# Optimization experiments

Hardware: AMD Instinct MI355X
Metric: run time of the kernel (lower is better)

## Reference

```python
import jax, jax.numpy as jnp
import numpy as np

T, E, DIM, HID = 8192, 8, 1024, 2048


def setup_inputs() -> dict:
    key = jax.random.key(0)
    k1, k2, k3 = jax.random.split(key, 3)
    x = jax.random.normal(k1, (T, DIM), dtype=jnp.float32)
    w1 = jax.random.normal(k2, (E, HID, DIM), dtype=jnp.float32)
    w2 = jax.random.normal(k3, (E, DIM, HID), dtype=jnp.float32)
    # Tokens are pre-grouped by expert; counts must sum exactly to T.
    num_tokens_per_expert = jnp.full((E,), T // E, dtype=jnp.int32)
    return {"x": x, "w1": w1, "w2": w2, "num_tokens_per_expert": num_tokens_per_expert}


def reference(x, w1, w2, num_tokens_per_expert):
    # Faithful to torch._grouped_mm path: bf16 casts, two ragged grouped GEMMs,
    # result cast back to x.dtype.
    gs = num_tokens_per_expert.astype(jnp.int32)
    xb = x.astype(jnp.bfloat16)                                  # [T, dim]
    w1t = jnp.swapaxes(w1.astype(jnp.bfloat16), -2, -1)          # [E, dim, hid]
    w2t = jnp.swapaxes(w2.astype(jnp.bfloat16), -2, -1)          # [E, hid, dim]
    h = jax.lax.ragged_dot(xb, w1t, gs)                          # [T, hid] bf16
    out = jax.lax.ragged_dot(h, w2t, gs)                         # [T, dim] bf16
    return out.astype(x.dtype)
```

## Files before the change

kernel.cpp:

```cpp
#include <hip/hip_runtime.h>
#include <stdint.h>

#define T_TOK 8192
#define NEXP  8
#define DIMSZ 1024
#define HIDSZ 2048
#define BK    64

typedef __attribute__((ext_vector_type(4))) float f32x4;
typedef __attribute__((ext_vector_type(8))) short s16x8;


__device__ __forceinline__ uint16_t f2bf(float f) {
  uint32_t u = __builtin_bit_cast(uint32_t, f);
  u += 0x7fffu + ((u >> 16) & 1u);
  return (uint16_t)(u >> 16);
}

__device__ __forceinline__ void gload_lds16(const uint16_t* g, const uint16_t* lds_base) {
  __builtin_amdgcn_global_load_lds(
      (const __attribute__((address_space(1))) uint32_t*)(uintptr_t)g,
      (__attribute__((address_space(3))) uint32_t*)(uint32_t)(uintptr_t)lds_base,
      16, 0, 0);
}


__global__ void cvt_all(const float* __restrict__ x, const float* __restrict__ w1,
                        const float* __restrict__ w2, uint16_t* __restrict__ xb,
                        uint16_t* __restrict__ w1b, uint16_t* __restrict__ w2b,
                        const int* __restrict__ counts, int* __restrict__ offs,
                        int* __restrict__ toffs) {
  if (blockIdx.x == 0 && threadIdx.x == 0) {
    int s = 0, ts = 0;
    for (int e = 0; e < NEXP; ++e) {
      offs[e] = s; toffs[e] = ts;
      s += counts[e]; ts += (counts[e] + 127) >> 7;
    }
    offs[NEXP] = s; toffs[NEXP] = ts;
  }
  const int b = blockIdx.x;
  const float4* src; uint4* dst; size_t base;
  if (b < 512)       { src = (const float4*)x;  dst = (uint4*)xb;  base = (size_t)b * 2048; }
  else if (b < 1536) { src = (const float4*)w1; dst = (uint4*)w1b; base = (size_t)(b - 512) * 2048; }
  else               { src = (const float4*)w2; dst = (uint4*)w2b; base = (size_t)(b - 1536) * 2048; }

#pragma unroll
  for (int half = 0; half < 2; ++half) {
    const size_t u0 = base + (size_t)half * 1024 + threadIdx.x;
    float4 v[8];
#pragma unroll
    for (int j = 0; j < 4; ++j) {
      v[2 * j]     = src[2 * (u0 + j * 256)];
      v[2 * j + 1] = src[2 * (u0 + j * 256) + 1];
    }
#pragma unroll
    for (int j = 0; j < 4; ++j) {
      uint4 o;
      o.x = f2bf(v[2 * j].x)     | ((uint32_t)f2bf(v[2 * j].y) << 16);
      o.y = f2bf(v[2 * j].z)     | ((uint32_t)f2bf(v[2 * j].w) << 16);
      o.z = f2bf(v[2 * j + 1].x) | ((uint32_t)f2bf(v[2 * j + 1].y) << 16);
      o.w = f2bf(v[2 * j + 1].z) | ((uint32_t)f2bf(v[2 * j + 1].w) << 16);
      dst[u0 + j * 256] = o;
    }
  }
}

template <bool OUT_BF16>
__global__ __launch_bounds__(256, 4)
void gemm_grouped(const uint16_t* __restrict__ A, const uint16_t* __restrict__ B,
                  void* __restrict__ C, const int* __restrict__ offs,
                  const int* __restrict__ toffs, int N, int K,
                  int mgs, int ntg, int ngx) {
  __shared__ __align__(16) uint16_t As[128 * BK];
  __shared__ __align__(16) uint16_t Bs[128 * BK];

  const int xcd  = blockIdx.x & 7;
  const int slot = blockIdx.x >> 3;
  const int mg = xcd / ngx, ng = xcd % ngx;
  const int mtg = mg * mgs + slot % mgs;
  const int nt  = ng * ntg + slot / mgs;
  if (mtg >= toffs[NEXP]) return;
  int e = 0;
#pragma unroll
  for (int i = 1; i < NEXP; ++i) e += (toffs[i] <= mtg) ? 1 : 0;
  const int mt      = mtg - toffs[e];
  const int m_start = offs[e];
  const int m_count = offs[e + 1] - m_start;
  const int m0      = mt * 128;
  int valid_m = m_count - m0;
  if (valid_m > 128) valid_m = 128;
  const int n0 = nt * 128;

  const int tid  = threadIdx.x;
  const int lane = tid & 63;
  const int w    = tid >> 6;
  const int wm = w & 1, wn = w >> 1;

  const int srow = tid >> 3;
  const int gch  = (tid & 7) ^ (srow & 7);
  const uint16_t* gB = B + (size_t)e * N * K;
  const uint16_t* gA = A + (size_t)m_start * K;

  const uint16_t* aP[4];
  const uint16_t* bP[4];
#pragma unroll
  for (int q = 0; q < 4; ++q) {
    const int rq = q * 32 + srow;
    const int ar = m0 + (rq < valid_m ? rq : valid_m - 1);
    aP[q] = gA + (size_t)ar * K + gch * 8;
    bP[q] = gB + (size_t)(n0 + q * 32 + srow) * K + gch * 8;
  }

  const int fr = lane & 15;
  const int q4 = lane >> 4;
  const int pA0 = ((q4)     ^ (fr & 7)) * 8;
  const int pA1 = ((4 + q4) ^ (fr & 7)) * 8;

  f32x4 acc[4][4];
#pragma unroll
  for (int mi = 0; mi < 4; ++mi)
#pragma unroll
    for (int ni = 0; ni < 4; ++ni) acc[mi][ni] = (f32x4){0.f, 0.f, 0.f, 0.f};

  for (int k0 = 0; k0 < K; k0 += BK) {
    __syncthreads();
#pragma unroll
    for (int q = 0; q < 4; ++q) {
      gload_lds16(aP[q], As + q * 2048 + w * 512);
      gload_lds16(bP[q], Bs + q * 2048 + w * 512);
      aP[q] += BK; bP[q] += BK;
    }
    __syncthreads();

    s16x8 af[4][2], bf[4][2];
#pragma unroll
    for (int mi = 0; mi < 4; ++mi) {
      const int r = (wm * 64 + mi * 16 + fr) * BK;
      af[mi][0] = *(const s16x8*)&As[r + pA0];
      af[mi][1] = *(const s16x8*)&As[r + pA1];
    }
#pragma unroll
    for (int ni = 0; ni < 4; ++ni) {
      const int r = (wn * 64 + ni * 16 + fr) * BK;
      bf[ni][0] = *(const s16x8*)&Bs[r + pA0];
      bf[ni][1] = *(const s16x8*)&Bs[r + pA1];
    }
#pragma unroll
    for (int t = 0; t < 2; ++t)
#pragma unroll
      for (int mi = 0; mi < 4; ++mi)
#pragma unroll
        for (int ni = 0; ni < 4; ++ni)
          acc[mi][ni] = __builtin_amdgcn_mfma_f32_16x16x32_bf16(af[mi][t], bf[ni][t], acc[mi][ni], 0, 0, 0);
  }

  const int cq = (lane >> 4) * 4;
  const int cc = lane & 15;
#pragma unroll
  for (int mi = 0; mi < 4; ++mi) {
#pragma unroll
    for (int r = 0; r < 4; ++r) {
      const int rt = wm * 64 + mi * 16 + cq + r;
      if (rt < valid_m) {
        const size_t rowoff = (size_t)(m_start + m0 + rt) * N;
#pragma unroll
        for (int ni = 0; ni < 4; ++ni) {
          const int col = n0 + wn * 64 + ni * 16 + cc;
          const float v = acc[mi][ni][r];
          if (OUT_BF16) {
            ((uint16_t*)C)[rowoff + col] = f2bf(v);
          } else {
            const uint32_t bb = (uint32_t)f2bf(v) << 16;
            ((float*)C)[rowoff + col] = __builtin_bit_cast(float, bb);
          }
        }
      }
    }
  }
}


extern "C" void kernel_launch(void* const* d_in, const int* in_sizes, int n_in,
                              void* d_out, int out_size, void* d_ws, size_t ws_size,
                              hipStream_t stream) {
  const float* x  = (const float*)d_in[0];
  const float* w1 = (const float*)d_in[1];
  const float* w2 = (const float*)d_in[2];
  const int* cnt  = (const int*)d_in[3];
  float* out = (float*)d_out;

  char* ws = (char*)d_ws;
  uint16_t* xb  = (uint16_t*)(ws);
  uint16_t* w1b = (uint16_t*)(ws + 16777216);
  uint16_t* w2b = (uint16_t*)(ws + 50331648);
  uint16_t* h   = (uint16_t*)(ws + 83886080);
  int* offs     = (int*)(ws + 117440512);
  int* toffs    = offs + 9;

  cvt_all<<<2560, 256, 0, stream>>>(x, w1, w2, xb, w1b, w2b, cnt, offs, toffs);

  gemm_grouped<true><<<8 * 18 * 8, 256, 0, stream>>>(
      xb, w1b, (void*)h, offs, toffs, HIDSZ, DIMSZ, 18, 8, 2);

  gemm_grouped<false><<<8 * 9 * 8, 256, 0, stream>>>(
      h, w2b, (void*)out, offs, toffs, DIMSZ, HIDSZ, 9, 8, 1);
}
```

Baseline: 290.0 us.

## Fuse fp32-to-bf16 weight conversion into grouped GEMM B-tile loads

Result: slower. 316.6 us (+9.2%).

```diff
diff --git a/kernel.cpp b/kernel.cpp
--- a/kernel.cpp
+++ b/kernel.cpp
@@ -17,7 +17,19 @@
   return (uint16_t)(u >> 16);
 }
 
-__device__ __forceinline__ void gload_lds16(const uint16_t* g, const uint16_t* lds_base) {
+#if __has_builtin(__builtin_amdgcn_cvt_pk_bf16_f32)
+typedef __attribute__((ext_vector_type(2))) __bf16 bf16x2;
+__device__ __forceinline__ uint32_t pk2(float a, float b) {
+  bf16x2 r = __builtin_amdgcn_cvt_pk_bf16_f32(a, b);
+  return __builtin_bit_cast(uint32_t, r);
+}
+#else
+__device__ __forceinline__ uint32_t pk2(float a, float b) {
+  return (uint32_t)f2bf(a) | ((uint32_t)f2bf(b) << 16);
+}
+#endif
+
+__device__ __forceinline__ void gload_lds16(const void* g, const void* lds_base) {
   __builtin_amdgcn_global_load_lds(
       (const __attribute__((address_space(1))) uint32_t*)(uintptr_t)g,
       (__attribute__((address_space(3))) uint32_t*)(uint32_t)(uintptr_t)lds_base,
@@ -25,11 +37,9 @@
 }
 
 
-__global__ void cvt_all(const float* __restrict__ x, const float* __restrict__ w1,
-                        const float* __restrict__ w2, uint16_t* __restrict__ xb,
-                        uint16_t* __restrict__ w1b, uint16_t* __restrict__ w2b,
-                        const int* __restrict__ counts, int* __restrict__ offs,
-                        int* __restrict__ toffs) {
+__global__ void cvt_x(const float* __restrict__ x, uint16_t* __restrict__ xb,
+                      const int* __restrict__ counts, int* __restrict__ offs,
+                      int* __restrict__ toffs) {
   if (blockIdx.x == 0 && threadIdx.x == 0) {
     int s = 0, ts = 0;
     for (int e = 0; e < NEXP; ++e) {
@@ -38,12 +48,9 @@
     }
     offs[NEXP] = s; toffs[NEXP] = ts;
   }
-  const int b = blockIdx.x;
-  const float4* src; uint4* dst; size_t base;
-  if (b < 512)       { src = (const float4*)x;  dst = (uint4*)xb;  base = (size_t)b * 2048; }
-  else if (b < 1536) { src = (const float4*)w1; dst = (uint4*)w1b; base = (size_t)(b - 512) * 2048; }
-  else               { src = (const float4*)w2; dst = (uint4*)w2b; base = (size_t)(b - 1536) * 2048; }
-
+  const float4* src = (const float4*)x;
+  uint4* dst = (uint4*)xb;
+  const size_t base = (size_t)blockIdx.x * 2048;
 #pragma unroll
   for (int half = 0; half < 2; ++half) {
     const size_t u0 = base + (size_t)half * 1024 + threadIdx.x;
@@ -56,23 +63,23 @@
 #pragma unroll
     for (int j = 0; j < 4; ++j) {
       uint4 o;
-      o.x = f2bf(v[2 * j].x)     | ((uint32_t)f2bf(v[2 * j].y) << 16);
-      o.y = f2bf(v[2 * j].z)     | ((uint32_t)f2bf(v[2 * j].w) << 16);
-      o.z = f2bf(v[2 * j + 1].x) | ((uint32_t)f2bf(v[2 * j + 1].y) << 16);
-      o.w = f2bf(v[2 * j + 1].z) | ((uint32_t)f2bf(v[2 * j + 1].w) << 16);
+      o.x = pk2(v[2 * j].x,     v[2 * j].y);
+      o.y = pk2(v[2 * j].z,     v[2 * j].w);
+      o.z = pk2(v[2 * j + 1].x, v[2 * j + 1].y);
+      o.w = pk2(v[2 * j + 1].z, v[2 * j + 1].w);
       dst[u0 + j * 256] = o;
     }
   }
 }
 
 template <bool OUT_BF16>
-__global__ __launch_bounds__(256, 4)
-void gemm_grouped(const uint16_t* __restrict__ A, const uint16_t* __restrict__ B,
+__global__ __launch_bounds__(256, 3)
+void gemm_grouped(const uint16_t* __restrict__ A, const float* __restrict__ B,
                   void* __restrict__ C, const int* __restrict__ offs,
                   const int* __restrict__ toffs, int N, int K,
                   int mgs, int ntg, int ngx) {
   __shared__ __align__(16) uint16_t As[128 * BK];
-  __shared__ __align__(16) uint16_t Bs[128 * BK];
+  __shared__ __align__(16) float    Bs[128 * BK];
 
   const int xcd  = blockIdx.x & 7;
   const int slot = blockIdx.x >> 3;
@@ -96,25 +103,33 @@
   const int w    = tid >> 6;
   const int wm = w & 1, wn = w >> 1;
 
-  const int srow = tid >> 3;
-  const int gch  = (tid & 7) ^ (srow & 7);
-  const uint16_t* gB = B + (size_t)e * N * K;
+  const int aRow = tid >> 3;
+  const int aG   = (tid & 7) ^ (aRow & 7);
   const uint16_t* gA = A + (size_t)m_start * K;
-
   const uint16_t* aP[4];
-  const uint16_t* bP[4];
 #pragma unroll
   for (int q = 0; q < 4; ++q) {
-    const int rq = q * 32 + srow;
+    const int rq = q * 32 + aRow;
     const int ar = m0 + (rq < valid_m ? rq : valid_m - 1);
-    aP[q] = gA + (size_t)ar * K + gch * 8;
-    bP[q] = gB + (size_t)(n0 + q * 32 + srow) * K + gch * 8;
-  }
+    aP[q] = gA + (size_t)ar * K + aG * 8;
+  }
+
+  const int bRow = tid >> 4;
+  const int bG   = (tid & 15) ^ (bRow & 7);
+  const float* gB = B + (size_t)e * N * K;
+  const float* bP[8];
+#pragma unroll
+  for (int q = 0; q < 8; ++q)
+    bP[q] = gB + (size_t)(n0 + q * 16 + bRow) * K + bG * 4;
 
   const int fr = lane & 15;
   const int q4 = lane >> 4;
   const int pA0 = ((q4)     ^ (fr & 7)) * 8;
   const int pA1 = ((4 + q4) ^ (fr & 7)) * 8;
+  const int pB00 = ((2 * q4)     ^ (fr & 7)) * 4;
+  const int pB01 = ((2 * q4 + 1) ^ (fr & 7)) * 4;
+  const int pB10 = ((8 + 2 * q4)     ^ (fr & 7)) * 4;
+  const int pB11 = ((8 + 2 * q4 + 1) ^ (fr & 7)) * 4;
 
   f32x4 acc[4][4];
 #pragma unroll
@@ -126,9 +141,13 @@
     __syncthreads();
 #pragma unroll
     for (int q = 0; q < 4; ++q) {
-      gload_lds16(aP[q], As + q * 2048 + w * 512);
-      gload_lds16(bP[q], Bs + q * 2048 + w * 512);
-      aP[q] += BK; bP[q] += BK;
+      gload_lds16(aP[q], (const char*)As + q * 4096 + w * 1024);
+      aP[q] += BK;
+    }
+#pragma unroll
+    for (int q = 0; q < 8; ++q) {
+      gload_lds16(bP[q], (const char*)Bs + q * 4096 + w * 1024);
+      bP[q] += BK;
     }
     __syncthreads();
 
@@ -142,8 +161,16 @@
 #pragma unroll
     for (int ni = 0; ni < 4; ++ni) {
       const int r = (wn * 64 + ni * 16 + fr) * BK;
-      bf[ni][0] = *(const s16x8*)&Bs[r + pA0];
-      bf[ni][1] = *(const s16x8*)&Bs[r + pA1];
+      f32x4 c00 = *(const f32x4*)&Bs[r + pB00];
+      f32x4 c01 = *(const f32x4*)&Bs[r + pB01];
+      f32x4 c10 = *(const f32x4*)&Bs[r + pB10];
+      f32x4 c11 = *(const f32x4*)&Bs[r + pB11];
+      uint4 u0 = make_uint4(pk2(c00[0], c00[1]), pk2(c00[2], c00[3]),
+                            pk2(c01[0], c01[1]), pk2(c01[2], c01[3]));
+      uint4 u1 = make_uint4(pk2(c10[0], c10[1]), pk2(c10[2], c10[3]),
+                            pk2(c11[0], c11[1]), pk2(c11[2], c11[3]));
+      bf[ni][0] = __builtin_bit_cast(s16x8, u0);
+      bf[ni][1] = __builtin_bit_cast(s16x8, u1);
     }
 #pragma unroll
     for (int t = 0; t < 2; ++t)
@@ -190,18 +217,16 @@
   float* out = (float*)d_out;
 
   char* ws = (char*)d_ws;
-  uint16_t* xb  = (uint16_t*)(ws);
-  uint16_t* w1b = (uint16_t*)(ws + 16777216);
-  uint16_t* w2b = (uint16_t*)(ws + 50331648);
-  uint16_t* h   = (uint16_t*)(ws + 83886080);
-  int* offs     = (int*)(ws + 117440512);
-  int* toffs    = offs + 9;
-
-  cvt_all<<<2560, 256, 0, stream>>>(x, w1, w2, xb, w1b, w2b, cnt, offs, toffs);
+  uint16_t* xb = (uint16_t*)ws;
+  uint16_t* h  = (uint16_t*)(ws + 16777216);
+  int* offs    = (int*)(ws + 50331648);
+  int* toffs   = offs + 9;
+
+  cvt_x<<<512, 256, 0, stream>>>(x, xb, cnt, offs, toffs);
 
   gemm_grouped<true><<<8 * 18 * 8, 256, 0, stream>>>(
-      xb, w1b, (void*)h, offs, toffs, HIDSZ, DIMSZ, 18, 8, 2);
+      xb, w1, (void*)h, offs, toffs, HIDSZ, DIMSZ, 18, 8, 2);
 
   gemm_grouped<false><<<8 * 9 * 8, 256, 0, stream>>>(
-      h, w2b, (void*)out, offs, toffs, DIMSZ, HIDSZ, 9, 8, 1);
-}
+      h, w2, (void*)out, offs, toffs, DIMSZ, HIDSZ, 9, 8, 1);
+}
```
